# Kernel optimization log

Measured on AMD Instinct MI355X. Metric: run time of the kernel, lower is better.

The kernel has to match this reference:

```python
import jax, jax.numpy as jnp
import numpy as np

H = 256          # hidden_dim
T = 3            # number of agent types (hard-coded in module)
N = 24576        # total agents, contiguous by type
N3 = N // T      # agents per type


def _ln(x, s, b):
    mu = jnp.mean(x, -1, keepdims=True)
    v = jnp.var(x, -1, keepdims=True)
    return (x - mu) * jax.lax.rsqrt(v + 1e-5) * s + b


def setup_inputs() -> dict:
    key = jax.random.key(0)
    ks = jax.random.split(key, 20)
    def p(i, shape, scale=0.02):
        return jax.random.normal(ks[i], shape, jnp.float32) * scale
    inp = {}
    inp['agent_x'] = p(0, (N, H), 1.0)
    inp['lane_x'] = p(1, (N, H), 1.0)
    inp['poly_x'] = p(2, (N, H), 1.0)
    inp['l2a_src'] = jax.random.randint(ks[3], (N,), 0, N)
    inp['g2a_src'] = jax.random.randint(ks[4], (N,), 0, N)
    # other_src[s, d] = src agent of type s for dst agent d (types contiguous)
    inp['other_src'] = jax.random.randint(ks[5], (T, N), 0, N3) + (jnp.arange(T) * N3)[:, None]
    # per-agent-type params
    inp['self_W'] = p(6, (T, H, H)); inp['self_b'] = jnp.zeros((T, H))
    inp['out_W'] = p(7, (T, 4 * H, H)); inp['out_b'] = jnp.zeros((T, H))
    inp['ffn_ln_s'] = jnp.ones((T, H)); inp['ffn_ln_b'] = jnp.zeros((T, H))
    inp['ffn_w1'] = p(8, (T, H, 4 * H)); inp['ffn_b1'] = jnp.zeros((T, 4 * H))
    inp['ffn_w2'] = p(9, (T, 4 * H, H)); inp['ffn_b2'] = jnp.zeros((T, H))
    inp['ffn_w3'] = p(10, (T, H, 4 * H)); inp['ffn_b3'] = jnp.zeros((T, 4 * H))
    # shared edge MLPs (prenorm: LN -> w1 -> relu -> w2)
    inp['l2a_ln_s'] = jnp.ones((3 * H,)); inp['l2a_ln_b'] = jnp.zeros((3 * H,))
    inp['l2a_w1'] = p(11, (3 * H, 4 * H)); inp['l2a_b1'] = jnp.zeros((4 * H,))
    inp['l2a_w2'] = p(12, (4 * H, H)); inp['l2a_b2'] = jnp.zeros((H,))
    inp['g2a_ln_s'] = jnp.ones((2 * H,)); inp['g2a_ln_b'] = jnp.zeros((2 * H,))
    inp['g2a_w1'] = p(13, (2 * H, 4 * H)); inp['g2a_b1'] = jnp.zeros((4 * H,))
    inp['g2a_w2'] = p(14, (4 * H, H)); inp['g2a_b2'] = jnp.zeros((H,))
    # per-src-agent-type 'other' MLPs
    inp['oth_ln_s'] = jnp.ones((T, 3 * H)); inp['oth_ln_b'] = jnp.zeros((T, 3 * H))
    inp['oth_w1'] = p(15, (T, 3 * H, 4 * H)); inp['oth_b1'] = jnp.zeros((T, 4 * H))
    inp['oth_w2'] = p(16, (T, 4 * H, H)); inp['oth_b2'] = jnp.zeros((T, H))
    return inp


def reference(agent_x, lane_x, poly_x, self_W, self_b, out_W, out_b,
              ffn_ln_s, ffn_ln_b, ffn_w1, ffn_b1, ffn_w2, ffn_b2, ffn_w3, ffn_b3,
              l2a_ln_s, l2a_ln_b, l2a_w1, l2a_b1, l2a_w2, l2a_b2,
              g2a_ln_s, g2a_ln_b, g2a_w1, g2a_b1, g2a_w2, g2a_b2,
              oth_ln_s, oth_ln_b, oth_w1, oth_b1, oth_w2, oth_b2,
              l2a_src, g2a_src, other_src):
    x = agent_x.reshape(T, N3, H)                      # agents grouped by type
    # self branch: Linear + ReLU per type
    self_out = jax.nn.relu(jnp.einsum('tnh,thk->tnk', x, self_W) + self_b[:, None, :])
    # l2a edge MLP: cat([lane, agent, lane]) -> prenorm MLP (shared weights)
    lane_feat = lane_x[l2a_src].reshape(T, N3, H)
    l2a_in = jnp.concatenate([lane_feat, x, lane_feat], -1)      # [T,N3,3H]
    l2a_out = jax.nn.relu(_ln(l2a_in, l2a_ln_s, l2a_ln_b) @ l2a_w1 + l2a_b1) @ l2a_w2 + l2a_b2
    # g2a edge MLP: cat([polygon, agent])
    poly_feat = poly_x[g2a_src].reshape(T, N3, H)
    g2a_in = jnp.concatenate([poly_feat, x], -1)                 # [T,N3,2H]
    g2a_out = jax.nn.relu(_ln(g2a_in, g2a_ln_s, g2a_ln_b) @ g2a_w1 + g2a_b1) @ g2a_w2 + g2a_b2
    # agent-other-agent: per source-agent-type MLP, then aggregate over src types
    src_feat = agent_x[other_src].reshape(T, T, N3, H)           # [src_t, dst_t, N3, H]
    xb = jnp.broadcast_to(x[None], (T, T, N3, H))
    oth_in = jnp.concatenate([src_feat, xb, src_feat], -1)       # [s,t,n,3H]
    oth_n = _ln(oth_in, oth_ln_s[:, None, None, :], oth_ln_b[:, None, None, :])
    oth_h = jax.nn.relu(jnp.einsum('stnd,sdm->stnm', oth_n, oth_w1) + oth_b1[:, None, None, :])
    oth_out = jnp.einsum('stnm,smh->stnh', oth_h, oth_w2) + oth_b2[:, None, None, :]
    other_agg = oth_out.sum(0)                                   # [T,N3,H]
    # fuse 4 branches -> out_fc -> PositionwiseFeedForward -> residual
    fused = jnp.concatenate([self_out, l2a_out, g2a_out, other_agg], -1)  # [T,N3,4H]
    out = jnp.einsum('tnd,tdh->tnh', fused, out_W) + out_b[:, None, :]
    y = _ln(out, ffn_ln_s[:, None, :], ffn_ln_b[:, None, :])
    g = jax.nn.silu(jnp.einsum('tnh,thm->tnm', y, ffn_w1) + ffn_b1[:, None, :])
    u = jnp.einsum('tnh,thm->tnm', y, ffn_w3) + ffn_b3[:, None, :]
    out = out + jnp.einsum('tnm,tmh->tnh', g * u, ffn_w2) + ffn_b2[:, None, :]
    return (out + x).reshape(N, H)
```

## Files before the change

kernel.cpp:

```cpp
#include <hip/hip_runtime.h>
#include <hip/hip_bf16.h>

typedef __hip_bfloat16 bf16;
typedef __bf16 v8bf __attribute__((ext_vector_type(8)));
typedef float f32x4 __attribute__((ext_vector_type(4)));

#define N_AG 24576
#define N3 8192

struct __align__(8) bf4 { bf16 x, y, z, w; };
__device__ __forceinline__ bf4 mk4(float a, float b, float c, float d) {
  bf4 r{__float2bfloat16(a), __float2bfloat16(b), __float2bfloat16(c), __float2bfloat16(d)};
  return r;
}

enum {
  EPI_RELU_BIAS = 0,
  EPI_BIAS      = 1,
  EPI_ACC_INIT  = 2,
  EPI_ACC_ADD   = 3,
  EPI_FINAL     = 4,
  EPI_SILU      = 5,
  EPI_MUL       = 6,
  EPI_GLU       = 7
};

__device__ __forceinline__ void gl_lds16(const bf16* g, short* l) {
  __builtin_amdgcn_global_load_lds(
      (const __attribute__((address_space(1))) unsigned int*)g,
      (__attribute__((address_space(3))) unsigned int*)l, 16, 0, 0);
}

template<int EPI, int K, int LDA, int LDB>
__device__ __forceinline__
void gemm_body(const bf16* __restrict__ A,
               const bf16* __restrict__ Bt,
               const float* __restrict__ bias,
               float* __restrict__ accbuf,
               bf16* __restrict__ Cout, int ldc,
               const float* __restrict__ resid,
               float* __restrict__ CoutF,
               int Nc, int row0, int col0)
{
  __shared__ __align__(16) short As[2][128 * 32];
  __shared__ __align__(16) short Bs[2][128 * 32];

  const int tid  = threadIdx.x;
  const int lane = tid & 63;
  const int w    = tid >> 6;
  const int quad = lane >> 4;
  const int l15  = lane & 15;

  f32x4 acc[4][4];
  const f32x4 zero = {0.f, 0.f, 0.f, 0.f};
#pragma unroll
  for (int i = 0; i < 4; ++i)
#pragma unroll
    for (int j = 0; j < 4; ++j) acc[i][j] = zero;

  const int srow = (w << 5) + (lane >> 2);
  const int ss   = ((lane >> 2) & 3) ^ ((lane >> 4) & 1);
  const int sc   = ((lane & 3) ^ ss) << 3;
  const bf16* aG  = A  + (long)(row0 + srow) * LDA + sc;
  const bf16* aG2 = aG + (long)16 * LDA;
  const bf16* bG  = Bt + (long)(col0 + srow) * LDB + sc;
  const bf16* bG2 = bG + (long)16 * LDB;
  const int ldsOff = w * 1024;

  const int wr = (w >> 1) * 64;
  const int wc = (w & 1) * 64;
  const int fs = (l15 & 3) ^ ((l15 >> 2) & 1);

  gl_lds16(aG,  As[0] + ldsOff);
  gl_lds16(aG2, As[0] + ldsOff + 512);
  gl_lds16(bG,  Bs[0] + ldsOff);
  gl_lds16(bG2, Bs[0] + ldsOff + 512);
  __syncthreads();

#pragma unroll
  for (int k0 = 0; k0 < K; k0 += 32) {
    constexpr int unused = 0; (void)unused;
    const int cur = (k0 >> 5) & 1;
    const int nk = k0 + 32;
    if (nk < K) {
      short* An = As[cur ^ 1] + ldsOff;
      short* Bn = Bs[cur ^ 1] + ldsOff;
      gl_lds16(aG + nk,  An);
      gl_lds16(aG2 + nk, An + 512);
      gl_lds16(bG + nk,  Bn);
      gl_lds16(bG2 + nk, Bn + 512);
    }
    const short* Ac = As[cur];
    const short* Bc = Bs[cur];
    const int pc = (quad ^ fs) * 8;
    v8bf af[4], bfm[4];
#pragma unroll
    for (int i = 0; i < 4; ++i) {
      af[i]  = *(const v8bf*)&Ac[(wr + i * 16 + l15) * 32 + pc];
      bfm[i] = *(const v8bf*)&Bc[(wc + i * 16 + l15) * 32 + pc];
    }
#pragma unroll
    for (int i = 0; i < 4; ++i)
#pragma unroll
      for (int j = 0; j < 4; ++j)
        acc[i][j] = __builtin_amdgcn_mfma_f32_16x16x32_bf16(af[i], bfm[j], acc[i][j], 0, 0, 0);
    __syncthreads();
  }

  if constexpr (EPI == EPI_GLU) {
#pragma unroll
    for (int ct = 0; ct < 4; ct += 2) {
      const int colg = col0 + wc + ct * 16 + l15;
      const int hcol = ((colg >> 5) << 4) + (colg & 15);
      const float bg = bias[colg];
      const float bu = bias[colg + 16];
#pragma unroll
      for (int rt = 0; rt < 4; ++rt) {
#pragma unroll
        for (int i = 0; i < 4; ++i) {
          const int row = row0 + wr + rt * 16 + quad * 4 + i;
          const float vg = acc[rt][ct][i] + bg;
          const float vu = acc[rt][ct + 1][i] + bu;
          Cout[(long)row * ldc + hcol] =
              __float2bfloat16(vg / (1.f + expf(-vg)) * vu);
        }
      }
    }
  } else {
#pragma unroll
    for (int ct = 0; ct < 4; ++ct) {
      const int col = col0 + wc + ct * 16 + l15;
      const float bv = bias ? bias[col] : 0.f;
#pragma unroll
      for (int rt = 0; rt < 4; ++rt) {
#pragma unroll
        for (int i = 0; i < 4; ++i) {
          const int row = row0 + wr + rt * 16 + quad * 4 + i;
          float v = acc[rt][ct][i] + bv;
          if constexpr (EPI == EPI_RELU_BIAS) {
            Cout[(long)row * ldc + col] = __float2bfloat16(v > 0.f ? v : 0.f);
          } else if constexpr (EPI == EPI_BIAS) {
            Cout[(long)row * ldc + col] = __float2bfloat16(v);
          } else if constexpr (EPI == EPI_ACC_INIT) {
            accbuf[(long)row * Nc + col] = v;
          } else if constexpr (EPI == EPI_ACC_ADD) {
            accbuf[(long)row * Nc + col] += v;
          } else if constexpr (EPI == EPI_FINAL) {
            CoutF[(long)row * ldc + col] =
                accbuf[(long)row * Nc + col] + v + resid[(long)row * ldc + col];
          } else if constexpr (EPI == EPI_SILU) {
            Cout[(long)row * ldc + col] = __float2bfloat16(v / (1.f + expf(-v)));
          }
        }
      }
    }
  }
}

template<int EPI, int K, int LDA, int LDB>
__device__ __forceinline__
void gemm64_body(const bf16* __restrict__ A,
                 const bf16* __restrict__ Bt,
                 const float* __restrict__ bias,
                 float* __restrict__ accbuf,
                 bf16* __restrict__ Cout, int ldc,
                 const float* __restrict__ resid,
                 float* __restrict__ CoutF,
                 int Nc, int row0, int col0)
{
  __shared__ __align__(16) short As[2][64 * 32];
  __shared__ __align__(16) short Bs[2][64 * 32];

  const int tid  = threadIdx.x;
  const int lane = tid & 63;
  const int w    = tid >> 6;
  const int quad = lane >> 4;
  const int l15  = lane & 15;

  f32x4 acc[2][2];
  const f32x4 zero = {0.f, 0.f, 0.f, 0.f};
#pragma unroll
  for (int i = 0; i < 2; ++i)
#pragma unroll
    for (int j = 0; j < 2; ++j) acc[i][j] = zero;

  const int srow = (w << 4) + (lane >> 2);
  const int ss   = ((lane >> 2) & 3) ^ ((lane >> 4) & 1);
  const int sc   = ((lane & 3) ^ ss) << 3;
  const bf16* aG = A  + (long)(row0 + srow) * LDA + sc;
  const bf16* bG = Bt + (long)(col0 + srow) * LDB + sc;
  const int ldsOff = w * 512;

  const int wr = (w >> 1) * 32;
  const int wc = (w & 1) * 32;
  const int fs = (l15 & 3) ^ ((l15 >> 2) & 1);

  gl_lds16(aG, As[0] + ldsOff);
  gl_lds16(bG, Bs[0] + ldsOff);
  __syncthreads();

#pragma unroll
  for (int k0 = 0; k0 < K; k0 += 32) {
    const int cur = (k0 >> 5) & 1;
    const int nk = k0 + 32;
    if (nk < K) {
      gl_lds16(aG + nk, As[cur ^ 1] + ldsOff);
      gl_lds16(bG + nk, Bs[cur ^ 1] + ldsOff);
    }
    const short* Ac = As[cur];
    const short* Bc = Bs[cur];
    const int pc = (quad ^ fs) * 8;
    v8bf af[2], bfm[2];
#pragma unroll
    for (int i = 0; i < 2; ++i) {
      af[i]  = *(const v8bf*)&Ac[(wr + i * 16 + l15) * 32 + pc];
      bfm[i] = *(const v8bf*)&Bc[(wc + i * 16 + l15) * 32 + pc];
    }
#pragma unroll
    for (int i = 0; i < 2; ++i)
#pragma unroll
      for (int j = 0; j < 2; ++j)
        acc[i][j] = __builtin_amdgcn_mfma_f32_16x16x32_bf16(af[i], bfm[j], acc[i][j], 0, 0, 0);
    __syncthreads();
  }

#pragma unroll
  for (int ct = 0; ct < 2; ++ct) {
    const int col = col0 + wc + ct * 16 + l15;
    const float bv = bias ? bias[col] : 0.f;
#pragma unroll
    for (int rt = 0; rt < 2; ++rt) {
#pragma unroll
      for (int i = 0; i < 4; ++i) {
        const int row = row0 + wr + rt * 16 + quad * 4 + i;
        float v = acc[rt][ct][i] + bv;
        if constexpr (EPI == EPI_RELU_BIAS) {
          Cout[(long)row * ldc + col] = __float2bfloat16(v > 0.f ? v : 0.f);
        } else if constexpr (EPI == EPI_BIAS) {
          Cout[(long)row * ldc + col] = __float2bfloat16(v);
        } else if constexpr (EPI == EPI_ACC_INIT) {
          accbuf[(long)row * Nc + col] = v;
        } else if constexpr (EPI == EPI_ACC_ADD) {
          accbuf[(long)row * Nc + col] += v;
        } else if constexpr (EPI == EPI_FINAL) {
          CoutF[(long)row * ldc + col] =
              accbuf[(long)row * Nc + col] + v + resid[(long)row * ldc + col];
        }
      }
    }
  }
}

template<int EPI, int K, int LDA, int LDB>
__global__ __launch_bounds__(256)
void gemm_k(const bf16* __restrict__ A,
            const bf16* __restrict__ Bt, long bTs,
            const float* __restrict__ bias, long biasTs,
            float* __restrict__ accbuf,
            bf16* __restrict__ Cout, int ldc,
            const float* __restrict__ resid,
            float* __restrict__ CoutF,
            int Nc)
{
  const int row0 = blockIdx.x * 128;
  const int col0 = blockIdx.y * 128;
  const int t    = row0 >> 13;
  gemm_body<EPI, K, LDA, LDB>(A, Bt + (long)t * bTs,
                              bias ? bias + (long)t * biasTs : nullptr,
                              accbuf, Cout, ldc, resid, CoutF, Nc, row0, col0);
}

template<int EPI, int K, int LDA, int LDB>
__global__ __launch_bounds__(256)
void gemm64_k(const bf16* __restrict__ A,
              const bf16* __restrict__ Bt, long bTs,
              const float* __restrict__ bias, long biasTs,
              float* __restrict__ accbuf,
              bf16* __restrict__ Cout, int ldc,
              const float* __restrict__ resid,
              float* __restrict__ CoutF,
              int Nc)
{
  const int row0 = blockIdx.x * 64;
  const int col0 = blockIdx.y * 64;
  const int t    = row0 >> 13;
  gemm64_body<EPI, K, LDA, LDB>(A, Bt + (long)t * bTs,
                                bias ? bias + (long)t * biasTs : nullptr,
                                accbuf, Cout, ldc, resid, CoutF, Nc, row0, col0);
}

__global__ __launch_bounds__(256)
void w2m_k(const bf16* __restrict__ outwT, const bf16* __restrict__ w2c,
           bf16* __restrict__ w2m)
{
  const int z = blockIdx.z, b = z / 3, t = z % 3;
  const int j = (b == 0) ? 1 : (b == 1) ? 2 : 3;
  gemm64_body<EPI_BIAS, 256, 1024, 256>(
      outwT + (long)t * 262144 + j * 256,
      w2c + (long)b * 262144,
      nullptr, nullptr, w2m + (long)z * 262144, 1024,
      nullptr, nullptr, 1024,
      blockIdx.x * 64, blockIdx.y * 64);
}

__global__ __launch_bounds__(256)
void transpose_k(const float* __restrict__ src, bf16* __restrict__ dst,
                 int K, int Nc, long sB, long dB)
{
  __shared__ bf16 tile[32][33];
  const int b = blockIdx.z;
  const float* s = src + (long)b * sB;
  bf16* d = dst + (long)b * dB;
  const int kb = blockIdx.y * 32, nb = blockIdx.x * 32;
  const int tx = threadIdx.x & 31, ty = threadIdx.x >> 5;
#pragma unroll
  for (int i = 0; i < 32; i += 8)
    tile[ty + i][tx] = __float2bfloat16(s[(long)(kb + ty + i) * Nc + nb + tx]);
  __syncthreads();
#pragma unroll
  for (int i = 0; i < 32; i += 8)
    d[(long)(nb + ty + i) * K + kb + tx] = tile[tx][ty + i];
}

__global__ __launch_bounds__(256)
void transpose13_k(const float* __restrict__ w1, const float* __restrict__ w3,
                   bf16* __restrict__ dst)
{
  __shared__ bf16 tile[32][33];
  const int t  = blockIdx.z;
  const int n0 = blockIdx.x * 32;
  const int k0 = blockIdx.y * 32;
  const int gi = n0 >> 5;
  const int tx = threadIdx.x & 31, ty = threadIdx.x >> 5;
  const float* src = ((tx & 16) ? w3 : w1) + (long)t * 262144;
  const int c = 16 * gi + (tx & 15);
#pragma unroll
  for (int i = 0; i < 32; i += 8)
    tile[ty + i][tx] = __float2bfloat16(src[(long)(k0 + ty + i) * 1024 + c]);
  __syncthreads();
#pragma unroll
  for (int i = 0; i < 32; i += 8)
    dst[((long)t * 2048 + n0 + ty + i) * 256 + k0 + tx] = tile[tx][ty + i];
}

struct FoldP { const float* w1[5]; const float* ls[5]; };
__global__ __launch_bounds__(256)
void fold_w1_k(FoldP p, bf16* __restrict__ dst)
{
  __shared__ float tile[32][33];
  const int z = blockIdx.z;
  const float* w1 = p.w1[z];
  const float* ls = p.ls[z];
  bf16* d = dst + (long)z * 524288;
  const int n0 = blockIdx.x * 32, i0 = blockIdx.y * 32;
  const int tx = threadIdx.x & 31, ty = threadIdx.x >> 5;
  const bool three = (z != 1) && (i0 < 256);
#pragma unroll
  for (int ii = 0; ii < 32; ii += 8) {
    const int row = i0 + ty + ii;
    float v = ls[row] * w1[(long)row * 1024 + n0 + tx];
    if (three) v += ls[row + 512] * w1[(long)(row + 512) * 1024 + n0 + tx];
    tile[ty + ii][tx] = v;
  }
  __syncthreads();
#pragma unroll
  for (int ii = 0; ii < 32; ii += 8)
    d[(long)(n0 + ty + ii) * 512 + i0 + tx] = __float2bfloat16(tile[tx][ty + ii]);
}

struct BInitP { const float* b1[5]; const float* fb1; const float* fb3; };
__global__ __launch_bounds__(256)
void binit_k(BInitP p, float* __restrict__ B1F,
             const float* __restrict__ out_b, float* __restrict__ TB,
             float* __restrict__ B13)
{
  const int i = blockIdx.x * 256 + threadIdx.x;
  if (i < 5120) {
    B1F[i] = p.b1[i >> 10][i & 1023];
  } else if (i < 5888) {
    TB[i - 5120] = out_b[i - 5120];
  } else if (i < 12032) {
    const int idx = i - 5888;
    const int t = idx >> 11, n = idx & 2047;
    const int c = ((n >> 5) << 4) | (n & 15);
    B13[idx] = (n & 16) ? p.fb3[t * 1024 + c] : p.fb1[t * 1024 + c];
  }
}

struct B1P { const float* w1[5]; const float* lb[5]; int kin[5]; };
__global__ __launch_bounds__(256)
void b1f_add_k(B1P p, float* __restrict__ dst)
{
  const int z   = blockIdx.x;
  const int kin = p.kin[z];
  const int kpb = (kin + 31) >> 5;
  const int k0  = blockIdx.y * kpb;
  const int k1  = min(k0 + kpb, kin);
  const float* w1 = p.w1[z];
  const float* lb = p.lb[z];
  const int n = threadIdx.x;
  float a0 = 0.f, a1 = 0.f, a2 = 0.f, a3 = 0.f;
  for (int k = k0; k < k1; ++k) {
    const float l = lb[k];
    const float* row = w1 + (long)k * 1024;
    a0 += l * row[n];       a1 += l * row[n + 256];
    a2 += l * row[n + 512]; a3 += l * row[n + 768];
  }
  float* d = dst + z * 1024 + n;
  atomicAdd(d, a0);       atomicAdd(d + 256, a1);
  atomicAdd(d + 512, a2); atomicAdd(d + 768, a3);
}

__global__ __launch_bounds__(256)
void tbias_add_k(const float* __restrict__ outW,
                 const float* __restrict__ l2a_b2, const float* __restrict__ g2a_b2,
                 const float* __restrict__ oth_b2, float* __restrict__ dst)
{
  const int t = blockIdx.x, h = threadIdx.x;
  const float* W = outW + (long)t * 262144;
  const int c0 = blockIdx.y * 32;
  float acc = 0.f;
  for (int c = c0; c < c0 + 32; ++c) {
    acc += l2a_b2[c] * W[(256 + c) * 256 + h];
    acc += g2a_b2[c] * W[(512 + c) * 256 + h];
    acc += (oth_b2[c] + oth_b2[256 + c] + oth_b2[512 + c]) * W[(768 + c) * 256 + h];
  }
  atomicAdd(&dst[t * 256 + h], acc);
}

__global__ __launch_bounds__(256)
void cast_k(const float* __restrict__ src, bf16* __restrict__ dst)
{
  const long i = (long)blockIdx.x * 256 + threadIdx.x;
  const float4 v = ((const float4*)src)[i];
  ((bf4*)dst)[i] = mk4(v.x, v.y, v.z, v.w);
}

__device__ __forceinline__ void wave_reduce2(float& s, float& q) {
#pragma unroll
  for (int off = 32; off > 0; off >>= 1) {
    s += __shfl_xor(s, off, 64);
    q += __shfl_xor(q, off, 64);
  }
}

template<int THREE>
__global__ __launch_bounds__(256)
void ln_norm_k(const float* __restrict__ feat, const float* __restrict__ x,
               const int* __restrict__ srcIdx, bf16* __restrict__ out)
{
  const int w = threadIdx.x >> 6, lane = threadIdx.x & 63;
  const int r = blockIdx.x * 4 + w;
  const int src = srcIdx[r];
  const float4 f4 = ((const float4*)(feat + (long)src * 256))[lane];
  const float4 x4 = ((const float4*)(x + (long)r * 256))[lane];
  const float fw = THREE ? 2.f : 1.f;
  float s = fw * (f4.x + f4.y + f4.z + f4.w) + (x4.x + x4.y + x4.z + x4.w);
  float q = fw * (f4.x * f4.x + f4.y * f4.y + f4.z * f4.z + f4.w * f4.w) +
            (x4.x * x4.x + x4.y * x4.y + x4.z * x4.z + x4.w * x4.w);
  wave_reduce2(s, q);
  const float rD  = THREE ? (1.f / 768.f) : (1.f / 512.f);
  const float mu  = s * rD;
  const float var = q * rD - mu * mu;
  const float inv = rsqrtf(var + 1e-5f);
  bf4* o = (bf4*)(out + (long)r * 512);
  o[lane]      = mk4((f4.x - mu) * inv, (f4.y - mu) * inv,
                     (f4.z - mu) * inv, (f4.w - mu) * inv);
  o[64 + lane] = mk4((x4.x - mu) * inv, (x4.y - mu) * inv,
                     (x4.z - mu) * inv, (x4.w - mu) * inv);
}

__global__ __launch_bounds__(256)
void ln_cat3_k(const float* __restrict__ feat, const float* __restrict__ x,
               const int* __restrict__ srcIdx,
               const float* __restrict__ ls, const float* __restrict__ lb,
               bf16* __restrict__ out)
{
  const int w = threadIdx.x >> 6, lane = threadIdx.x & 63;
  const int r = blockIdx.x * 4 + w;
  const int src = srcIdx[r];
  const float4 f4 = ((const float4*)(feat + (long)src * 256))[lane];
  const float4 x4 = ((const float4*)(x + (long)r * 256))[lane];
  float s = 2.f * (f4.x + f4.y + f4.z + f4.w) + (x4.x + x4.y + x4.z + x4.w);
  float q = 2.f * (f4.x * f4.x + f4.y * f4.y + f4.z * f4.z + f4.w * f4.w) +
            (x4.x * x4.x + x4.y * x4.y + x4.z * x4.z + x4.w * x4.w);
  wave_reduce2(s, q);
  const float mu  = s * (1.f / 768.f);
  const float var = q * (1.f / 768.f) - mu * mu;
  const float inv = rsqrtf(var + 1e-5f);
  const float4 s0 = ((const float4*)ls)[lane],         b0 = ((const float4*)lb)[lane];
  const float4 s1 = ((const float4*)(ls + 256))[lane], b1 = ((const float4*)(lb + 256))[lane];
  const float4 s2 = ((const float4*)(ls + 512))[lane], b2 = ((const float4*)(lb + 512))[lane];
  bf4* o = (bf4*)(out + (long)r * 768);
  o[lane] = mk4((f4.x - mu) * inv * s0.x + b0.x, (f4.y - mu) * inv * s0.y + b0.y,
                (f4.z - mu) * inv * s0.z + b0.z, (f4.w - mu) * inv * s0.w + b0.w);
  o[64 + lane] = mk4((x4.x - mu) * inv * s1.x + b1.x, (x4.y - mu) * inv * s1.y + b1.y,
                     (x4.z - mu) * inv * s1.z + b1.z, (x4.w - mu) * inv * s1.w + b1.w);
  o[128 + lane] = mk4((f4.x - mu) * inv * s2.x + b2.x, (f4.y - mu) * inv * s2.y + b2.y,
                      (f4.z - mu) * inv * s2.z + b2.z, (f4.w - mu) * inv * s2.w + b2.w);
}

__global__ __launch_bounds__(256)
void ln_cat2_k(const float* __restrict__ feat, const float* __restrict__ x,
               const int* __restrict__ srcIdx,
               const float* __restrict__ ls, const float* __restrict__ lb,
               bf16* __restrict__ out)
{
  const int w = threadIdx.x >> 6, lane = threadIdx.x & 63;
  const int r = blockIdx.x * 4 + w;
  const int src = srcIdx[r];
  const float4 f4 = ((const float4*)(feat + (long)src * 256))[lane];
  const float4 x4 = ((const float4*)(x + (long)r * 256))[lane];
  float s = (f4.x + f4.y + f4.z + f4.w) + (x4.x + x4.y + x4.z + x4.w);
  float q = (f4.x * f4.x + f4.y * f4.y + f4.z * f4.z + f4.w * f4.w) +
            (x4.x * x4.x + x4.y * x4.y + x4.z * x4.z + x4.w * x4.w);
  wave_reduce2(s, q);
  const float mu  = s * (1.f / 512.f);
  const float var = q * (1.f / 512.f) - mu * mu;
  const float inv = rsqrtf(var + 1e-5f);
  const float4 s0 = ((const float4*)ls)[lane],         b0 = ((const float4*)lb)[lane];
  const float4 s1 = ((const float4*)(ls + 256))[lane], b1 = ((const float4*)(lb + 256))[lane];
  bf4* o = (bf4*)(out + (long)r * 512);
  o[lane] = mk4((f4.x - mu) * inv * s0.x + b0.x, (f4.y - mu) * inv * s0.y + b0.y,
                (f4.z - mu) * inv * s0.z + b0.z, (f4.w - mu) * inv * s0.w + b0.w);
  o[64 + lane] = mk4((x4.x - mu) * inv * s1.x + b1.x, (x4.y - mu) * inv * s1.y + b1.y,
                     (x4.z - mu) * inv * s1.z + b1.z, (x4.w - mu) * inv * s1.w + b1.w);
}

__global__ __launch_bounds__(256)
void ln_ffn_k(const float* __restrict__ ob, const float* __restrict__ ls,
              const float* __restrict__ lb, bf16* __restrict__ y, long lsStride)
{
  const int w = threadIdx.x >> 6, lane = threadIdx.x & 63;
  const int r = blockIdx.x * 4 + w;
  const long po = (long)(r >> 13) * lsStride;
  const float4 v4 = ((const float4*)(ob + (long)r * 256))[lane];
  float s = v4.x + v4.y + v4.z + v4.w;
  float q = v4.x * v4.x + v4.y * v4.y + v4.z * v4.z + v4.w * v4.w;
  wave_reduce2(s, q);
  const float mu  = s * (1.f / 256.f);
  const float var = q * (1.f / 256.f) - mu * mu;
  const float inv = rsqrtf(var + 1e-5f);
  const float4 s0 = ((const float4*)(ls + po))[lane];
  const float4 b0 = ((const float4*)(lb + po))[lane];
  ((bf4*)(y + (long)r * 256))[lane] =
      mk4((v4.x - mu) * inv * s0.x + b0.x, (v4.y - mu) * inv * s0.y + b0.y,
          (v4.z - mu) * inv * s0.z + b0.z, (v4.w - mu) * inv * s0.w + b0.w);
}

__global__ __launch_bounds__(256)
void silu_mul_k(bf16* __restrict__ g, const bf16* __restrict__ u)
{
  const long i = (long)blockIdx.x * 256 + threadIdx.x;
  const bf4 g4 = ((const bf4*)g)[i];
  const bf4 u4 = ((const bf4*)u)[i];
  float a = __bfloat162float(g4.x), b = __bfloat162float(g4.y);
  float c = __bfloat162float(g4.z), d = __bfloat162float(g4.w);
  a = a / (1.f + expf(-a)) * __bfloat162float(u4.x);
  b = b / (1.f + expf(-b)) * __bfloat162float(u4.y);
  c = c / (1.f + expf(-c)) * __bfloat162float(u4.z);
  d = d / (1.f + expf(-d)) * __bfloat162float(u4.w);
  ((bf4*)g)[i] = mk4(a, b, c, d);
}

__global__ __launch_bounds__(256)
void fill_k(float* __restrict__ p, int n)
{
  const int i = blockIdx.x * 256 + threadIdx.x;
  if (i < n) p[i] = 2.0f;
}

extern "C" void kernel_launch(void* const* d_in, const int* in_sizes, int n_in,
                              void* d_out, int out_size, void* d_ws, size_t ws_size,
                              hipStream_t stream)
{
  const float* agent_x  = (const float*)d_in[0];
  const float* lane_x   = (const float*)d_in[1];
  const float* poly_x   = (const float*)d_in[2];
  const int*   l2a_src  = (const int*)d_in[3];
  const int*   g2a_src  = (const int*)d_in[4];
  const int*   other_src= (const int*)d_in[5];
  const float* self_W   = (const float*)d_in[6];
  const float* self_b   = (const float*)d_in[7];
  const float* out_W    = (const float*)d_in[8];
  const float* out_b    = (const float*)d_in[9];
  const float* ffn_ln_s = (const float*)d_in[10];
  const float* ffn_ln_b = (const float*)d_in[11];
  const float* ffn_w1   = (const float*)d_in[12];
  const float* ffn_b1   = (const float*)d_in[13];
  const float* ffn_w2   = (const float*)d_in[14];
  const float* ffn_b2   = (const float*)d_in[15];
  const float* ffn_w3   = (const float*)d_in[16];
  const float* ffn_b3   = (const float*)d_in[17];
  const float* l2a_ln_s = (const float*)d_in[18];
  const float* l2a_ln_b = (const float*)d_in[19];
  const float* l2a_w1   = (const float*)d_in[20];
  const float* l2a_b1   = (const float*)d_in[21];
  const float* l2a_w2   = (const float*)d_in[22];
  const float* l2a_b2   = (const float*)d_in[23];
  const float* g2a_ln_s = (const float*)d_in[24];
  const float* g2a_ln_b = (const float*)d_in[25];
  const float* g2a_w1   = (const float*)d_in[26];
  const float* g2a_b1   = (const float*)d_in[27];
  const float* g2a_w2   = (const float*)d_in[28];
  const float* g2a_b2   = (const float*)d_in[29];
  const float* oth_ln_s = (const float*)d_in[30];
  const float* oth_ln_b = (const float*)d_in[31];
  const float* oth_w1   = (const float*)d_in[32];
  const float* oth_b1   = (const float*)d_in[33];
  const float* oth_w2   = (const float*)d_in[34];
  const float* oth_b2   = (const float*)d_in[35];

  float* outp = (float*)d_out;
  const dim3 B256(256);

  const size_t TIER_A = 135707648;
  const size_t TIER_C = 12058624;

  if (ws_size >= TIER_A) {
    char* base = (char*)d_ws;
    bf16* wT = (bf16*)base;
    const long SELF_WT = 0,       OUT_WT  = 196608,  FFN_W13T = 983040;
    const long FFN_W2T = 2555904;
    const long W2C = 3342336,     W1F     = 4653056, W2M      = 7274496;
    float* B1F  = (float*)(base + 22413312L);
    float* TB   = (float*)(base + 22433792L);
    float* B13  = (float*)(base + 22436864L);
    bf16*  nbuf = (bf16*)(base + 22461440L);
    bf16*  h1   = (bf16*)(base + 47627264L);
    float* oF   = (float*)(base + 97958912L);
    bf16*  ybuf = (bf16*)(base + 123124736L);
    bf16*  xbf  = h1;

    auto TRB = [&](const float* s, long dOff, int K, int Nc, long sB, long dB, int b) {
      transpose_k<<<dim3(Nc / 32, K / 32, b), B256, 0, stream>>>(s, wT + dOff, K, Nc, sB, dB);
    };
    TRB(self_W, SELF_WT, 256, 256,  65536, 65536, 3);
    TRB(out_W,  OUT_WT,  1024, 256, 262144, 262144, 3);
    TRB(ffn_w2, FFN_W2T, 1024, 256, 262144, 262144, 3);
    transpose13_k<<<dim3(64, 8, 3), B256, 0, stream>>>(ffn_w1, ffn_w3, wT + FFN_W13T);
    cast_k<<<256, B256, 0, stream>>>(l2a_w2, wT + W2C);
    cast_k<<<256, B256, 0, stream>>>(g2a_w2, wT + W2C + 262144);
    cast_k<<<768, B256, 0, stream>>>(oth_w2, wT + W2C + 524288);

    FoldP fp = {{l2a_w1, g2a_w1, oth_w1, oth_w1 + 786432, oth_w1 + 1572864},
                {l2a_ln_s, g2a_ln_s, oth_ln_s, oth_ln_s + 768, oth_ln_s + 1536}};
    fold_w1_k<<<dim3(32, 16, 5), B256, 0, stream>>>(fp, wT + W1F);

    BInitP ip = {{l2a_b1, g2a_b1, oth_b1, oth_b1 + 1024, oth_b1 + 2048}, ffn_b1, ffn_b3};
    binit_k<<<47, B256, 0, stream>>>(ip, B1F, out_b, TB, B13);
    B1P bp = {{l2a_w1, g2a_w1, oth_w1, oth_w1 + 786432, oth_w1 + 1572864},
              {l2a_ln_b, g2a_ln_b, oth_ln_b, oth_ln_b + 768, oth_ln_b + 1536},
              {768, 512, 768, 768, 768}};
    b1f_add_k<<<dim3(5, 32), B256, 0, stream>>>(bp, B1F);
    tbias_add_k<<<dim3(3, 8), B256, 0, stream>>>(out_W, l2a_b2, g2a_b2, oth_b2, TB);
    w2m_k<<<dim3(4, 16, 15), B256, 0, stream>>>(wT + OUT_WT, wT + W2C, wT + W2M);

    const dim3 Gw1(N_AG / 128, 8), Gglu(N_AG / 128, 16);
    const dim3 G64(N_AG / 64, 4);

    cast_k<<<N_AG / 4, B256, 0, stream>>>(agent_x, xbf);
    gemm64_k<EPI_RELU_BIAS, 256, 256, 256><<<G64, B256, 0, stream>>>(
        xbf, wT + SELF_WT, 65536, self_b, 256,
        nullptr, ybuf, 256, nullptr, nullptr, 256);
    gemm64_k<EPI_ACC_INIT, 256, 256, 1024><<<G64, B256, 0, stream>>>(
        ybuf, wT + OUT_WT, 262144, TB, 256,
        oF, nullptr, 0, nullptr, nullptr, 256);

    for (int b = 0; b < 5; ++b) {
      const int* src = (b == 0) ? l2a_src : (b == 1) ? g2a_src
                                          : other_src + (long)(b - 2) * N_AG;
      const float* feat = (b == 0) ? lane_x : (b == 1) ? poly_x : agent_x;
      if (b == 1) ln_norm_k<0><<<N_AG / 4, B256, 0, stream>>>(feat, agent_x, src, nbuf);
      else        ln_norm_k<1><<<N_AG / 4, B256, 0, stream>>>(feat, agent_x, src, nbuf);
      gemm_k<EPI_RELU_BIAS, 512, 512, 512><<<Gw1, B256, 0, stream>>>(
          nbuf, wT + W1F + (long)b * 524288, 0, B1F + b * 1024, 0,
          nullptr, h1, 1024, nullptr, nullptr, 1024);
      gemm64_k<EPI_ACC_ADD, 1024, 1024, 1024><<<G64, B256, 0, stream>>>(
          h1, wT + W2M + (long)b * 786432, 262144, nullptr, 0,
          oF, nullptr, 0, nullptr, nullptr, 256);
    }

    ln_ffn_k<<<N_AG / 4, B256, 0, stream>>>(oF, ffn_ln_s, ffn_ln_b, ybuf, 256);
    gemm_k<EPI_GLU, 256, 256, 256><<<Gglu, B256, 0, stream>>>(
        ybuf, wT + FFN_W13T, 524288, B13, 2048,
        nullptr, h1, 1024, nullptr, nullptr, 2048);
    gemm64_k<EPI_FINAL, 1024, 1024, 1024><<<G64, B256, 0, stream>>>(
        h1, wT + FFN_W2T, 262144, ffn_b2, 256,
        oF, nullptr, 256, agent_x, outp, 256);
    return;
  }

  if (ws_size < TIER_C) {
    fill_k<<<(out_size + 255) / 256, B256, 0, stream>>>(outp, out_size);
    return;
  }

  const int CH = 2048;
  char* base = (char*)d_ws;
  bf16*  wt     = (bf16*)base;
  bf16*  nbuf   = (bf16*)(base + 1572864L);
  bf16*  bbuf   = (bf16*)(base + 4718592L);
  bf16*  h1     = (bf16*)(base + 5767168L);
  float* outF32 = (float*)(base + 9961472L);
  bf16*  ybuf   = (bf16*)(base + 524288L);
  bf16*  xbf    = h1;
  bf16*  g_pre  = h1;
  bf16*  u_pre  = nbuf;

  const dim3 Gw1(CH / 128, 8), Gw2(CH / 128, 2);
  auto TR = [&](const float* s, int K, int Nc) {
    transpose_k<<<dim3(Nc / 32, K / 32), B256, 0, stream>>>(s, wt, K, Nc, 0, 0);
  };

  for (int t = 0; t < 3; ++t) {
    for (int c = 0; c < N3 / CH; ++c) {
      const long r0 = (long)t * N3 + (long)c * CH;
      const float* xC   = agent_x + r0 * 256;
      float*       outC = outp + r0 * 256;

      cast_k<<<CH / 4, B256, 0, stream>>>(xC, xbf);
      TR(self_W + (long)t * 65536, 256, 256);
      gemm_k<EPI_RELU_BIAS, 256, 256, 256><<<Gw2, B256, 0, stream>>>(
          xbf, wt, 0, self_b + t * 256, 0, nullptr, bbuf, 256,
          nullptr, nullptr, 256);
      TR(out_W + (long)t * 262144 + 0 * 65536, 256, 256);
      gemm_k<EPI_ACC_INIT, 256, 256, 256><<<Gw2, B256, 0, stream>>>(
          bbuf, wt, 0, out_b + t * 256, 0, outF32, nullptr, 0,
          nullptr, nullptr, 256);

      ln_cat3_k<<<CH / 4, B256, 0, stream>>>(lane_x, xC, l2a_src + r0,
                                             l2a_ln_s, l2a_ln_b, nbuf);
      TR(l2a_w1, 768, 1024);
      gemm_k<EPI_RELU_BIAS, 768, 768, 768><<<Gw1, B256, 0, stream>>>(
          nbuf, wt, 0, l2a_b1, 0, nullptr, h1, 1024,
          nullptr, nullptr, 1024);
      TR(l2a_w2, 1024, 256);
      gemm_k<EPI_BIAS, 1024, 1024, 1024><<<Gw2, B256, 0, stream>>>(
          h1, wt, 0, l2a_b2, 0, nullptr, bbuf, 256,
          nullptr, nullptr, 256);
      TR(out_W + (long)t * 262144 + 1 * 65536, 256, 256);
      gemm_k<EPI_ACC_ADD, 256, 256, 256><<<Gw2, B256, 0, stream>>>(
          bbuf, wt, 0, nullptr, 0, outF32, nullptr, 0,
          nullptr, nullptr, 256);

      ln_cat2_k<<<CH / 4, B256, 0, stream>>>(poly_x, xC, g2a_src + r0,
                                             g2a_ln_s, g2a_ln_b, nbuf);
      TR(g2a_w1, 512, 1024);
      gemm_k<EPI_RELU_BIAS, 512, 512, 512><<<Gw1, B256, 0, stream>>>(
          nbuf, wt, 0, g2a_b1, 0, nullptr, h1, 1024,
          nullptr, nullptr, 1024);
      TR(g2a_w2, 1024, 256);
      gemm_k<EPI_BIAS, 1024, 1024, 1024><<<Gw2, B256, 0, stream>>>(
          h1, wt, 0, g2a_b2, 0, nullptr, bbuf, 256,
          nullptr, nullptr, 256);
      TR(out_W + (long)t * 262144 + 2 * 65536, 256, 256);
      gemm_k<EPI_ACC_ADD, 256, 256, 256><<<Gw2, B256, 0, stream>>>(
          bbuf, wt, 0, nullptr, 0, outF32, nullptr, 0,
          nullptr, nullptr, 256);

      for (int s = 0; s < 3; ++s) {
        ln_cat3_k<<<CH / 4, B256, 0, stream>>>(
            agent_x, xC, other_src + (long)s * N_AG + r0,
            oth_ln_s + s * 768, oth_ln_b + s * 768, nbuf);
        TR(oth_w1 + (long)s * 786432, 768, 1024);
        gemm_k<EPI_RELU_BIAS, 768, 768, 768><<<Gw1, B256, 0, stream>>>(
            nbuf, wt, 0, oth_b1 + s * 1024, 0, nullptr, h1, 1024,
            nullptr, nullptr, 1024);
        TR(oth_w2 + (long)s * 262144, 1024, 256);
        gemm_k<EPI_BIAS, 1024, 1024, 1024><<<Gw2, B256, 0, stream>>>(
            h1, wt, 0, oth_b2 + s * 256, 0, nullptr, bbuf, 256,
            nullptr, nullptr, 256);
        TR(out_W + (long)t * 262144 + 3 * 65536, 256, 256);
        gemm_k<EPI_ACC_ADD, 256, 256, 256><<<Gw2, B256, 0, stream>>>(
            bbuf, wt, 0, nullptr, 0, outF32, nullptr, 0,
            nullptr, nullptr, 256);
      }

      ln_ffn_k<<<CH / 4, B256, 0, stream>>>(outF32, ffn_ln_s + t * 256,
                                            ffn_ln_b + t * 256, ybuf, 0);
      TR(ffn_w1 + (long)t * 262144, 256, 1024);
      gemm_k<EPI_BIAS, 256, 256, 256><<<Gw1, B256, 0, stream>>>(
          ybuf, wt, 0, ffn_b1 + t * 1024, 0, nullptr, g_pre, 1024,
          nullptr, nullptr, 1024);
      TR(ffn_w3 + (long)t * 262144, 256, 1024);
      gemm_k<EPI_BIAS, 256, 256, 256><<<Gw1, B256, 0, stream>>>(
          ybuf, wt, 0, ffn_b3 + t * 1024, 0, nullptr, u_pre, 1024,
          nullptr, nullptr, 1024);
      silu_mul_k<<<CH, B256, 0, stream>>>(g_pre, u_pre);
      TR(ffn_w2 + (long)t * 262144, 1024, 256);
      gemm_k<EPI_FINAL, 1024, 1024, 1024><<<Gw2, B256, 0, stream>>>(
          g_pre, wt, 0, ffn_b2 + t * 256, 0, outF32, nullptr, 256,
          xC, outC, 1024);
    }
  }
}
```

Before: 815.4 us.

## Triple-buffer GEMM LDS tiles with explicit vmcnt waits for deeper prefetch

Both GEMM bodies move from double- to triple-buffered LDS staging. Tile loads are issued two k-steps ahead, and explicit s_waitcnt vmcnt plus s_barrier sequences wait only for the tile about to be consumed, so global loads stay in flight across iterations. The aim is to hide more global-to-LDS latency behind MFMA work. The cost is 50% more LDS per block, which may lower occupancy, and the hand-written waitcnt values depend on the compiler not reordering or adding other vector memory ops inside the loop.

```diff
diff --git a/kernel.cpp b/kernel.cpp
--- a/kernel.cpp
+++ b/kernel.cpp
@@ -31,6 +31,16 @@
       (__attribute__((address_space(3))) unsigned int*)l, 16, 0, 0);
 }
 
+__device__ __forceinline__ void wait_vm_barrier(int pending) {
+  if (pending == 8)      asm volatile("s_waitcnt vmcnt(8)\ns_barrier" ::: "memory");
+  else if (pending == 4) asm volatile("s_waitcnt vmcnt(4)\ns_barrier" ::: "memory");
+  else if (pending == 2) asm volatile("s_waitcnt vmcnt(2)\ns_barrier" ::: "memory");
+  else                   asm volatile("s_waitcnt vmcnt(0)\ns_barrier" ::: "memory");
+}
+__device__ __forceinline__ void lgkm_barrier() {
+  asm volatile("s_waitcnt lgkmcnt(0)\ns_barrier" ::: "memory");
+}
+
 template<int EPI, int K, int LDA, int LDB>
 __device__ __forceinline__
 void gemm_body(const bf16* __restrict__ A,
@@ -42,8 +52,8 @@
                float* __restrict__ CoutF,
                int Nc, int row0, int col0)
 {
-  __shared__ __align__(16) short As[2][128 * 32];
-  __shared__ __align__(16) short Bs[2][128 * 32];
+  __shared__ __align__(16) short As[3][128 * 32];
+  __shared__ __align__(16) short Bs[3][128 * 32];
 
   const int tid  = threadIdx.x;
   const int lane = tid & 63;
@@ -71,27 +81,32 @@
   const int wc = (w & 1) * 64;
   const int fs = (l15 & 3) ^ ((l15 >> 2) & 1);
 
-  gl_lds16(aG,  As[0] + ldsOff);
-  gl_lds16(aG2, As[0] + ldsOff + 512);
-  gl_lds16(bG,  Bs[0] + ldsOff);
-  gl_lds16(bG2, Bs[0] + ldsOff + 512);
-  __syncthreads();
-
-#pragma unroll
-  for (int k0 = 0; k0 < K; k0 += 32) {
-    constexpr int unused = 0; (void)unused;
-    const int cur = (k0 >> 5) & 1;
-    const int nk = k0 + 32;
-    if (nk < K) {
-      short* An = As[cur ^ 1] + ldsOff;
-      short* Bn = Bs[cur ^ 1] + ldsOff;
+  constexpr int NT = K / 32;
+
+  gl_lds16(aG,       As[0] + ldsOff);
+  gl_lds16(aG2,      As[0] + ldsOff + 512);
+  gl_lds16(bG,       Bs[0] + ldsOff);
+  gl_lds16(bG2,      Bs[0] + ldsOff + 512);
+  gl_lds16(aG + 32,  As[1] + ldsOff);
+  gl_lds16(aG2 + 32, As[1] + ldsOff + 512);
+  gl_lds16(bG + 32,  Bs[1] + ldsOff);
+  gl_lds16(bG2 + 32, Bs[1] + ldsOff + 512);
+
+#pragma unroll
+  for (int t = 0; t < NT; ++t) {
+    const int nk = (t + 2) * 32;
+    if (t + 2 < NT) {
+      short* An = As[(t + 2) % 3] + ldsOff;
+      short* Bn = Bs[(t + 2) % 3] + ldsOff;
       gl_lds16(aG + nk,  An);
       gl_lds16(aG2 + nk, An + 512);
       gl_lds16(bG + nk,  Bn);
       gl_lds16(bG2 + nk, Bn + 512);
     }
-    const short* Ac = As[cur];
-    const short* Bc = Bs[cur];
+    wait_vm_barrier((t + 2 < NT) ? 8 : ((t + 1 < NT) ? 4 : 0));
+
+    const short* Ac = As[t % 3];
+    const short* Bc = Bs[t % 3];
     const int pc = (quad ^ fs) * 8;
     v8bf af[4], bfm[4];
 #pragma unroll
@@ -104,7 +119,7 @@
 #pragma unroll
       for (int j = 0; j < 4; ++j)
         acc[i][j] = __builtin_amdgcn_mfma_f32_16x16x32_bf16(af[i], bfm[j], acc[i][j], 0, 0, 0);
-    __syncthreads();
+    lgkm_barrier();
   }
 
   if constexpr (EPI == EPI_GLU) {
@@ -168,8 +183,8 @@
                  float* __restrict__ CoutF,
                  int Nc, int row0, int col0)
 {
-  __shared__ __align__(16) short As[2][64 * 32];
-  __shared__ __align__(16) short Bs[2][64 * 32];
+  __shared__ __align__(16) short As[3][64 * 32];
+  __shared__ __align__(16) short Bs[3][64 * 32];
 
   const int tid  = threadIdx.x;
   const int lane = tid & 63;
@@ -195,20 +210,24 @@
   const int wc = (w & 1) * 32;
   const int fs = (l15 & 3) ^ ((l15 >> 2) & 1);
 
-  gl_lds16(aG, As[0] + ldsOff);
-  gl_lds16(bG, Bs[0] + ldsOff);
-  __syncthreads();
-
-#pragma unroll
-  for (int k0 = 0; k0 < K; k0 += 32) {
-    const int cur = (k0 >> 5) & 1;
-    const int nk = k0 + 32;
-    if (nk < K) {
-      gl_lds16(aG + nk, As[cur ^ 1] + ldsOff);
-      gl_lds16(bG + nk, Bs[cur ^ 1] + ldsOff);
+  constexpr int NT = K / 32;
+
+  gl_lds16(aG,      As[0] + ldsOff);
+  gl_lds16(bG,      Bs[0] + ldsOff);
+  gl_lds16(aG + 32, As[1] + ldsOff);
+  gl_lds16(bG + 32, Bs[1] + ldsOff);
+
+#pragma unroll
+  for (int t = 0; t < NT; ++t) {
+    const int nk = (t + 2) * 32;
+    if (t + 2 < NT) {
+      gl_lds16(aG + nk, As[(t + 2) % 3] + ldsOff);
+      gl_lds16(bG + nk, Bs[(t + 2) % 3] + ldsOff);
     }
-    const short* Ac = As[cur];
-    const short* Bc = Bs[cur];
+    wait_vm_barrier((t + 2 < NT) ? 4 : ((t + 1 < NT) ? 2 : 0));
+
+    const short* Ac = As[t % 3];
+    const short* Bc = Bs[t % 3];
     const int pc = (quad ^ fs) * 8;
     v8bf af[2], bfm[2];
 #pragma unroll
@@ -221,7 +240,7 @@
 #pragma unroll
       for (int j = 0; j < 2; ++j)
         acc[i][j] = __builtin_amdgcn_mfma_f32_16x16x32_bf16(af[i], bfm[j], acc[i][j], 0, 0, 0);
-    __syncthreads();
+    lgkm_barrier();
   }
 
 #pragma unroll
```

Result: no change. 811.5 us (-0.5%).
